# Kernel tuning notes

Measured on AMD Instinct MI355X. Metric: run time of the kernel, lower is better.

The kernel has to match this reference:

```python
import jax, jax.numpy as jnp
import numpy as np

N = 20000       # nodes
C = 64          # channels per irrep
E = 320000      # edges (avg degree 16)
S = 64          # num_species
R = 8           # radial embedding dim
HR = 64         # radial MLP hidden
HEADS = 2       # readout heads
AVG = 16.0      # avg_num_neighbors
SOFT = 2.0      # soft_normalization


def setup_inputs() -> dict:
    key = jax.random.key(0)
    ks = jax.random.split(key, 28)
    g = lambda k, sh, sc=1.0: jax.random.normal(k, sh, dtype=jnp.float32) * sc
    inv = lambda n: 1.0 / float(np.sqrt(n))
    return {
        "edge_vectors": g(ks[0], (E, 3)),
        "node_feats_s": g(ks[1], (N, C)),
        "node_feats_v": g(ks[2], (N, C, 3)),
        "radial_embeddings": g(ks[3], (E, R)),
        "node_species": jax.random.randint(ks[4], (N,), 0, S),
        "senders": jax.random.randint(ks[5], (E,), 0, N),
        "receivers": jax.random.randint(ks[6], (E,), 0, N),
        # residual FullyConnectedTensorProduct(feats, one-hot species) weights
        "W_rs": g(ks[7], (S, C, C), inv(C)),
        "W_rv": g(ks[8], (S, C, C), inv(C)),
        # interaction: linear up, radial MLP (5 TP paths), linear down
        "W_up_s": g(ks[9], (C, C), inv(C)),
        "W_up_v": g(ks[10], (C, C), inv(C)),
        "Wr1": g(ks[11], (R, HR), inv(R)),
        "Wr2": g(ks[12], (HR, 5 * C), inv(HR)),
        "W_down_s": g(ks[13], (C, C), inv(C)),
        "W_down_v": g(ks[14], (C, C), inv(C)),
        # equivariant product basis: per-channel species-indexed symmetric-contraction weights
        "w1s": g(ks[15], (S, C)),
        "w1v": g(ks[16], (S, C)),
        "w2ss": g(ks[17], (S, C)),
        "w2vv": g(ks[18], (S, C)),
        "w2sv": g(ks[19], (S, C)),
        "W_prod_s": g(ks[20], (C, C), inv(C)),
        "W_prod_v": g(ks[21], (C, C), inv(C)),
        # linear readout heads (out_irreps -> 1x0e per head)
        "w_read": g(ks[22], (HEADS, C), inv(C)),
    }


def reference(edge_vectors, node_feats_s, node_feats_v, radial_embeddings,
              node_species, senders, receivers,
              W_rs, W_rv, W_up_s, W_up_v, Wr1, Wr2, W_down_s, W_down_v,
              w1s, w1v, w2ss, w2vv, w2sv, W_prod_s, W_prod_v, w_read):
    n_nodes = node_feats_s.shape[0]
    sp = node_species

    # --- residual connection: FCTP(feats, one-hot(species)) == species-indexed channel mix
    res_s = jnp.einsum('nc,ncd->nd', node_feats_s, W_rs[sp])
    res_v = jnp.einsum('ncx,ncd->ndx', node_feats_v, W_rv[sp])

    # --- InteractionBlock ---
    s_u = node_feats_s @ W_up_s
    v_u = jnp.einsum('ncx,cd->ndx', node_feats_v, W_up_v)
    nrm = jnp.linalg.norm(edge_vectors, axis=-1, keepdims=True)
    u = edge_vectors / jnp.maximum(nrm, 1e-9)  # l=1 spherical harmonic direction [E,3]
    # radial MLP -> per-edge per-channel weights for the 5 CG paths of (0e+1o)x(0e+1o)->0e+1o
    w = (jax.nn.silu(radial_embeddings @ Wr1) @ Wr2).reshape(-1, 5, s_u.shape[1])
    se = s_u[senders]            # [E,C] gather (irregular)
    ve = v_u[senders]            # [E,C,3]
    dot = jnp.einsum('ecx,ex->ec', ve, u)          # 1o x 1o -> 0e
    crs = jnp.cross(ve, u[:, None, :])             # 1o x 1o -> 1o
    m_s = w[:, 0] * se + w[:, 3] * dot
    m_v = (w[:, 1][..., None] * ve
           + w[:, 2][..., None] * u[:, None, :]
           + w[:, 4][..., None] * crs)
    a_s = jax.ops.segment_sum(m_s, receivers, num_segments=n_nodes) / AVG
    a_v = jax.ops.segment_sum(m_v, receivers, num_segments=n_nodes) / AVG
    a_s = a_s @ W_down_s
    a_v = jnp.einsum('ncx,cd->ndx', a_v, W_down_v)

    # --- EquivariantProductBasisBlock: symmetric contraction (correlation<=2), per-channel
    # species-indexed weights, followed by a linear to out_irreps ---
    vv = jnp.sum(a_v * a_v, axis=-1)                                   # 1o (x) 1o -> 0e
    p_s = w1s[sp] * a_s + w2ss[sp] * a_s * a_s + w2vv[sp] * vv
    p_v = w1v[sp][..., None] * a_v + w2sv[sp][..., None] * a_s[..., None] * a_v
    p_s = p_s @ W_prod_s
    p_v = jnp.einsum('ncx,cd->ndx', p_v, W_prod_v)

    # --- soft normalization: phi(n) = 1/(1 + n*sus(n)), n = norm/SOFT ---
    def sus(x):
        return jnp.where(x > 0, jnp.exp(-1.0 / jnp.where(x > 0, x, 1.0)), 0.0)

    def phi(n):
        n = n / SOFT
        return 1.0 / (1.0 + n * sus(n))

    f_s = p_s * phi(jnp.abs(p_s))
    f_v = p_v * phi(jnp.linalg.norm(p_v, axis=-1, keepdims=True))

    # --- residual add ---
    f_s = f_s + res_s
    f_v = f_v + res_v

    # --- readout heads (Linear out_irreps -> 1x0e), stacked on axis=1 ---
    node_out = jnp.einsum('nc,hc->nh', f_s, w_read)
    return (node_out, f_s, f_v)
```

## Files before the change

### kernel.cpp

```cpp
#include <hip/hip_runtime.h>

#define N_NODES 20000
#define C 64
#define E_EDGES 320000
#define S_SPEC 64
#define R_DIM 8
#define HR 64
#define HEADS 2
#define TE 128
#define NT (E_EDGES/TE)
#define HPAD 68
#define INV_AVG (1.0f/16.0f)

#define FS_OFF 40000
#define FV_OFF 1320000

typedef short bf16x4 __attribute__((ext_vector_type(4)));
typedef float f32x4  __attribute__((ext_vector_type(4)));

__device__ __forceinline__ unsigned short f2bf(float f){
  unsigned u = __float_as_uint(f);
  u += 0x7fffu + ((u >> 16) & 1u);
  return (unsigned short)(u >> 16);
}
__device__ __forceinline__ float bf2f(unsigned short b){
  return __uint_as_float(((unsigned)b) << 16);
}
__device__ __forceinline__ float phi_f(float x){
  float n = x * 0.5f;
  float s = (n > 0.0f) ? expf(-1.0f/n) : 0.0f;
  return 1.0f / (1.0f + n * s);
}

__global__ __launch_bounds__(256) void wr2t_kernel(const float* __restrict__ Wr2,
                                                   unsigned short* __restrict__ wr2t){
  int idx = blockIdx.x*256 + threadIdx.x;
  int n = idx >> 6, k = idx & 63;
  wr2t[idx] = f2bf(Wr2[k*320 + n] * INV_AVG);
}

__global__ __launch_bounds__(256) void node_up_kernel(
    const float* __restrict__ fs, const float* __restrict__ fv,
    const float* __restrict__ Wus, const float* __restrict__ Wuv,
    ushort4* __restrict__ suv){
  const int ni = threadIdx.x >> 6;
  const int d  = threadIdx.x & 63;
  const int n  = blockIdx.x*4 + ni;
  __shared__ float s_l[4][C];
  __shared__ float v_l[4][3][C];
  s_l[ni][d] = fs[n*C + d];
  #pragma unroll
  for (int x = 0; x < 3; ++x) v_l[ni][x][d] = fv[(n*C + d)*3 + x];
  __syncthreads();
  float as = 0.f, a0 = 0.f, a1 = 0.f, a2 = 0.f;
  #pragma unroll 4
  for (int c = 0; c < C; ++c){
    float wsv = Wus[c*C + d];
    float wvv = Wuv[c*C + d];
    as += s_l[ni][c] * wsv;
    a0 += v_l[ni][0][c] * wvv;
    a1 += v_l[ni][1][c] * wvv;
    a2 += v_l[ni][2][c] * wvv;
  }
  ushort4 o;
  o.x = f2bf(as); o.y = f2bf(a0); o.z = f2bf(a1); o.w = f2bf(a2);
  suv[(size_t)n*C + d] = o;
}

__global__ __launch_bounds__(256) void hist_kernel(const int* __restrict__ rcv, int* __restrict__ count){
  int e = blockIdx.x*256 + threadIdx.x;
  atomicAdd(&count[rcv[e]], 1);
}

__global__ __launch_bounds__(1024) void scan_kernel(const int* __restrict__ count, int* __restrict__ cursor){
  __shared__ int sums[1024];
  const int t = threadIdx.x;
  const int base = t*20;
  int s = 0;
  #pragma unroll 4
  for (int i = 0; i < 20; ++i){ int idx = base+i; if (idx < N_NODES) s += count[idx]; }
  sums[t] = s;
  __syncthreads();
  for (int off = 1; off < 1024; off <<= 1){
    int v = (t >= off) ? sums[t-off] : 0;
    __syncthreads();
    sums[t] += v;
    __syncthreads();
  }
  int run = (t > 0) ? sums[t-1] : 0;
  for (int i = 0; i < 20; ++i){
    int idx = base+i;
    if (idx < N_NODES){ cursor[idx] = run; run += count[idx]; }
  }
}

__global__ __launch_bounds__(256) void scatter_kernel(
    const int* __restrict__ snd, const int* __restrict__ rcv,
    const float* __restrict__ ev, const float* __restrict__ re,
    int* __restrict__ cursor,
    int* __restrict__ snd_s, int* __restrict__ rcv_s,
    float4* __restrict__ u_s, float* __restrict__ re_s){
  int e = blockIdx.x*256 + threadIdx.x;
  int r = rcv[e];
  int pos = atomicAdd(&cursor[r], 1);
  snd_s[pos] = snd[e];
  rcv_s[pos] = r;
  float x = ev[e*3+0], y = ev[e*3+1], z = ev[e*3+2];
  float nr = sqrtf(x*x + y*y + z*z);
  float inv = 1.0f / fmaxf(nr, 1e-9f);
  float4 u4; u4.x = x*inv; u4.y = y*inv; u4.z = z*inv; u4.w = 0.f;
  u_s[pos] = u4;
  const float4* rp = (const float4*)&re[(size_t)e*R_DIM];
  float4 ra = rp[0], rb = rp[1];
  float4* op = (float4*)&re_s[(size_t)pos*R_DIM];
  op[0] = ra; op[1] = rb;
}

__global__ __launch_bounds__(512, 4) void edge_kernel(
    const float4* __restrict__ u_s, const float* __restrict__ re_s,
    const int* __restrict__ snd_s, const int* __restrict__ rcv_s,
    const float* __restrict__ Wr1, const unsigned short* __restrict__ wr2t,
    const ushort4* __restrict__ suv,
    float* __restrict__ a_s, float* __restrict__ a_v)
{
  __shared__ __align__(16) float Wr1_l[R_DIM*HR];
  __shared__ __align__(16) unsigned short Wr2T_l[320*HPAD];
  __shared__ __align__(16) unsigned short h_l[TE*HPAD];
  __shared__ __align__(16) float4 u_l[TE];
  __shared__ int snd_l[TE];
  __shared__ int rcv_l[TE];

  const int t = threadIdx.x;
  const int lane = t & 63;
  const int w = t >> 6;
  int b = blockIdx.x;
  int xcd = b & 7, idx = b >> 3;
  const int q = NT >> 3, r = NT & 7;
  int tile = (xcd < r ? xcd*(q+1) : r*(q+1) + (xcd-r)*q) + idx;
  const int e0 = tile * TE;

  Wr1_l[t] = Wr1[t];
  #pragma unroll
  for (int j = 0; j < 10; ++j){
    int i4 = t + 512*j;
    ushort4 v4 = ((const ushort4*)wr2t)[i4];
    int el = i4*4; int n = el >> 6, k = el & 63;
    *(ushort4*)&Wr2T_l[n*HPAD + k] = v4;
  }
  if (t < TE){
    int e = e0 + t;
    u_l[t] = u_s[e];
    snd_l[t] = snd_s[e];
    rcv_l[t] = rcv_s[e];
  }
  __syncthreads();

  const int cl = lane & 15;
  const int ebase = w*16 + (lane >> 4)*4;
  ushort4 gv[4][4];
  #pragma unroll
  for (int i = 0; i < 4; ++i){
    const ushort4* sp_ = &suv[(size_t)snd_l[ebase + i]*C];
    #pragma unroll
    for (int k2 = 0; k2 < 4; ++k2) gv[i][k2] = sp_[k2*16 + cl];
  }

  {
    int e = t & 127, qh = t >> 7;
    const float4* rp = (const float4*)&re_s[(size_t)(e0 + e)*R_DIM];
    float4 ra = rp[0], rb = rp[1];
    unsigned short hh[16];
    #pragma unroll
    for (int kk = 0; kk < 16; ++kk){
      int k = qh*16 + kk;
      float acc = ra.x*Wr1_l[0*HR+k] + ra.y*Wr1_l[1*HR+k] + ra.z*Wr1_l[2*HR+k] + ra.w*Wr1_l[3*HR+k]
                + rb.x*Wr1_l[4*HR+k] + rb.y*Wr1_l[5*HR+k] + rb.z*Wr1_l[6*HR+k] + rb.w*Wr1_l[7*HR+k];
      hh[kk] = f2bf(acc / (1.0f + expf(-acc)));
    }
    #pragma unroll
    for (int j4 = 0; j4 < 4; ++j4)
      *(ushort4*)&h_l[e*HPAD + qh*16 + j4*4] = *(ushort4*)&hh[j4*4];
  }
  __syncthreads();

  f32x4 acc[20];
  #pragma unroll
  for (int cf = 0; cf < 20; ++cf) acc[cf] = (f32x4){0.f,0.f,0.f,0.f};
  {
    const int arow = (w*16 + (lane & 15))*HPAD;
    const int koff = 4*(lane >> 4);
    #pragma unroll
    for (int kt = 0; kt < 4; ++kt){
      bf16x4 af = *(const bf16x4*)&h_l[arow + kt*16 + koff];
      #pragma unroll
      for (int cf = 0; cf < 20; ++cf){
        bf16x4 bf = *(const bf16x4*)&Wr2T_l[(cf*16 + (lane & 15))*HPAD + kt*16 + koff];
        acc[cf] = __builtin_amdgcn_mfma_f32_16x16x16bf16_1k(af, bf, acc[cf], 0, 0, 0);
      }
    }
  }

  {
    float ms[4], mv0[4], mv1[4], mv2[4];
    #pragma unroll
    for (int k2 = 0; k2 < 4; ++k2){ ms[k2]=0.f; mv0[k2]=0.f; mv1[k2]=0.f; mv2[k2]=0.f; }
    int cur = rcv_l[ebase];
    #pragma unroll
    for (int i = 0; i < 4; ++i){
      int el = ebase + i;
      int rc = rcv_l[el];
      if (rc != cur){
        #pragma unroll
        for (int k2 = 0; k2 < 4; ++k2){
          int c = k2*16 + cl;
          unsafeAtomicAdd(&a_s[cur*C + c],       ms[k2]);
          unsafeAtomicAdd(&a_v[(cur*3+0)*C + c], mv0[k2]);
          unsafeAtomicAdd(&a_v[(cur*3+1)*C + c], mv1[k2]);
          unsafeAtomicAdd(&a_v[(cur*3+2)*C + c], mv2[k2]);
          ms[k2]=0.f; mv0[k2]=0.f; mv1[k2]=0.f; mv2[k2]=0.f;
        }
        cur = rc;
      }
      float u0 = u_l[el].x, u1 = u_l[el].y, u2 = u_l[el].z;
      #pragma unroll
      for (int k2 = 0; k2 < 4; ++k2){
        float se  = bf2f(gv[i][k2].x);
        float ve0 = bf2f(gv[i][k2].y);
        float ve1 = bf2f(gv[i][k2].z);
        float ve2 = bf2f(gv[i][k2].w);
        float w0 = acc[0*4+k2][i];
        float w1 = acc[1*4+k2][i];
        float w2 = acc[2*4+k2][i];
        float w3 = acc[3*4+k2][i];
        float w4 = acc[4*4+k2][i];
        float dt  = ve0*u0 + ve1*u1 + ve2*u2;
        float cr0 = ve1*u2 - ve2*u1;
        float cr1 = ve2*u0 - ve0*u2;
        float cr2 = ve0*u1 - ve1*u0;
        ms[k2]  += w0*se + w3*dt;
        mv0[k2] += w1*ve0 + w2*u0 + w4*cr0;
        mv1[k2] += w1*ve1 + w2*u1 + w4*cr1;
        mv2[k2] += w1*ve2 + w2*u2 + w4*cr2;
      }
    }
    #pragma unroll
    for (int k2 = 0; k2 < 4; ++k2){
      int c = k2*16 + cl;
      unsafeAtomicAdd(&a_s[cur*C + c],       ms[k2]);
      unsafeAtomicAdd(&a_v[(cur*3+0)*C + c], mv0[k2]);
      unsafeAtomicAdd(&a_v[(cur*3+1)*C + c], mv1[k2]);
      unsafeAtomicAdd(&a_v[(cur*3+2)*C + c], mv2[k2]);
    }
  }
}

__global__ __launch_bounds__(256) void node_post_kernel(
    const float* __restrict__ a_s, const float* __restrict__ a_v,
    const float* __restrict__ fs_in, const float* __restrict__ fv_in,
    const int* __restrict__ species,
    const float* __restrict__ W_rs, const float* __restrict__ W_rv,
    const float* __restrict__ W_ds, const float* __restrict__ W_dv,
    const float* __restrict__ w1s, const float* __restrict__ w1v,
    const float* __restrict__ w2ss, const float* __restrict__ w2vv, const float* __restrict__ w2sv,
    const float* __restrict__ W_ps, const float* __restrict__ W_pv,
    const float* __restrict__ w_read, float* __restrict__ out)
{
  const int ni = threadIdx.x >> 6;
  const int d  = threadIdx.x & 63;
  const int n  = blockIdx.x*4 + ni;
  const int sp = species[n];
  __shared__ float as_l[4][C];
  __shared__ float av_l[4][3][C];
  __shared__ float si_l[4][C];
  __shared__ float vi_l[4][3][C];
  as_l[ni][d] = a_s[n*C + d];
  #pragma unroll
  for (int x=0;x<3;x++) av_l[ni][x][d] = a_v[(n*3+x)*C + d];
  si_l[ni][d] = fs_in[n*C + d];
  #pragma unroll
  for (int x=0;x<3;x++) vi_l[ni][x][d] = fv_in[(n*C + d)*3 + x];
  __syncthreads();
  const float* Wrs_p = W_rs + sp*C*C;
  const float* Wrv_p = W_rv + sp*C*C;
  float bs=0, bv0=0, bv1=0, bv2=0, rs=0, rv0=0, rv1=0, rv2=0;
  for (int c=0;c<C;++c){
    float wds = W_ds[c*C+d], wdv = W_dv[c*C+d];
    float wrs = Wrs_p[c*C+d], wrv = Wrv_p[c*C+d];
    bs  += as_l[ni][c]*wds;
    bv0 += av_l[ni][0][c]*wdv; bv1 += av_l[ni][1][c]*wdv; bv2 += av_l[ni][2][c]*wdv;
    rs  += si_l[ni][c]*wrs;
    rv0 += vi_l[ni][0][c]*wrv; rv1 += vi_l[ni][1][c]*wrv; rv2 += vi_l[ni][2][c]*wrv;
  }
  float vv = bv0*bv0 + bv1*bv1 + bv2*bv2;
  float ps  = w1s[sp*C+d]*bs + w2ss[sp*C+d]*bs*bs + w2vv[sp*C+d]*vv;
  float c1v = w1v[sp*C+d], c2sv = w2sv[sp*C+d];
  float pv0 = c1v*bv0 + c2sv*bs*bv0;
  float pv1 = c1v*bv1 + c2sv*bs*bv1;
  float pv2 = c1v*bv2 + c2sv*bs*bv2;
  __syncthreads();
  as_l[ni][d] = ps; av_l[ni][0][d]=pv0; av_l[ni][1][d]=pv1; av_l[ni][2][d]=pv2;
  __syncthreads();
  float qs=0, qv0=0, qv1=0, qv2=0;
  for (int c=0;c<C;++c){
    float wps = W_ps[c*C+d], wpv = W_pv[c*C+d];
    qs  += as_l[ni][c]*wps;
    qv0 += av_l[ni][0][c]*wpv; qv1 += av_l[ni][1][c]*wpv; qv2 += av_l[ni][2][c]*wpv;
  }
  float fsv = qs * phi_f(fabsf(qs)) + rs;
  float nv = sqrtf(qv0*qv0 + qv1*qv1 + qv2*qv2);
  float ph = phi_f(nv);
  float fv0 = qv0*ph + rv0;
  float fv1 = qv1*ph + rv1;
  float fv2 = qv2*ph + rv2;
  out[FS_OFF + n*C + d] = fsv;
  float* fvo = &out[FV_OFF + (size_t)(n*C + d)*3];
  fvo[0]=fv0; fvo[1]=fv1; fvo[2]=fv2;
  #pragma unroll
  for (int h=0; h<HEADS; ++h){
    float r = fsv * w_read[h*C + d];
    #pragma unroll
    for (int off=32; off>0; off>>=1) r += __shfl_down(r, off);
    if (d == 0) out[n*HEADS + h] = r;
  }
}

extern "C" void kernel_launch(void* const* d_in, const int* in_sizes, int n_in,
                              void* d_out, int out_size, void* d_ws, size_t ws_size,
                              hipStream_t stream)
{
  const float* ev   = (const float*)d_in[0];
  const float* nfs  = (const float*)d_in[1];
  const float* nfv  = (const float*)d_in[2];
  const float* re   = (const float*)d_in[3];
  const int*   spec = (const int*)d_in[4];
  const int*   snd  = (const int*)d_in[5];
  const int*   rcv  = (const int*)d_in[6];
  const float* W_rs = (const float*)d_in[7];
  const float* W_rv = (const float*)d_in[8];
  const float* Wus  = (const float*)d_in[9];
  const float* Wuv  = (const float*)d_in[10];
  const float* Wr1  = (const float*)d_in[11];
  const float* Wr2  = (const float*)d_in[12];
  const float* Wds  = (const float*)d_in[13];
  const float* Wdv  = (const float*)d_in[14];
  const float* w1s  = (const float*)d_in[15];
  const float* w1v  = (const float*)d_in[16];
  const float* w2ss = (const float*)d_in[17];
  const float* w2vv = (const float*)d_in[18];
  const float* w2sv = (const float*)d_in[19];
  const float* Wps  = (const float*)d_in[20];
  const float* Wpv  = (const float*)d_in[21];
  const float* wrd  = (const float*)d_in[22];

  float* out = (float*)d_out;
  float* ws  = (float*)d_ws;
  ushort4* suv  = (ushort4*)ws;
  float*   a_s  = ws + 2560000;
  float*   a_v  = ws + 3840000;
  int*    count = (int*)(ws + 7680000);
  int*    cursr = (int*)(ws + 7700000);
  int*    snd_s = (int*)(ws + 7720000);
  int*    rcv_s = (int*)(ws + 8040000);
  float4* u_s   = (float4*)(ws + 8360000);
  float*  re_s  = ws + 9640000;
  unsigned short* wr2t = (unsigned short*)(ws + 12200000);

  hipMemsetAsync(a_s, 0, (size_t)5120000*sizeof(float), stream);
  hipMemsetAsync(count, 0, (size_t)N_NODES*sizeof(int), stream);

  wr2t_kernel<<<(320*64)/256, 256, 0, stream>>>(Wr2, wr2t);
  node_up_kernel<<<N_NODES/4, 256, 0, stream>>>(nfs, nfv, Wus, Wuv, suv);
  hist_kernel<<<E_EDGES/256, 256, 0, stream>>>(rcv, count);
  scan_kernel<<<1, 1024, 0, stream>>>(count, cursr);
  scatter_kernel<<<E_EDGES/256, 256, 0, stream>>>(snd, rcv, ev, re, cursr,
                                                  snd_s, rcv_s, u_s, re_s);
  edge_kernel<<<NT, 512, 0, stream>>>(u_s, re_s, snd_s, rcv_s, Wr1, wr2t,
                                      suv, a_s, a_v);
  node_post_kernel<<<N_NODES/4, 256, 0, stream>>>(a_s, a_v, nfs, nfv, spec,
      W_rs, W_rv, Wds, Wdv, w1s, w1v, w2ss, w2vv, w2sv, Wps, Wpv, wrd, out);
}
```

Before: 433.9 us.

## Aggregate edge messages per receiver segment in LDS before global atomics

Edges within a tile, already sorted by receiver, are grouped into receiver segments with a block-wide prefix scan. Each thread reduces its partial messages into a shared-memory slot per segment using LDS atomics, and one flush then issues a single global atomic per segment and channel. Segments past the slot limit still fall back to direct global atomics. The radial MLP hidden layer is now computed directly in registers as MFMA A-fragments, dropping the h_l staging buffer and one barrier. In exchange the kernel adds a serial scan with several barriers, extra LDS (about 24 KB of accumulators) that may lower occupancy, and LDS atomic contention.

Result: faster. 411.2 us (-5.2%).

```diff
diff --git a/kernel.cpp b/kernel.cpp
--- a/kernel.cpp
+++ b/kernel.cpp
@@ -10,6 +10,7 @@
 #define TE 128
 #define NT (E_EDGES/TE)
 #define HPAD 68
+#define NSLOT 24
 #define INV_AVG (1.0f/16.0f)
 
 #define FS_OFF 40000
@@ -125,10 +126,14 @@
 {
   __shared__ __align__(16) float Wr1_l[R_DIM*HR];
   __shared__ __align__(16) unsigned short Wr2T_l[320*HPAD];
-  __shared__ __align__(16) unsigned short h_l[TE*HPAD];
+  __shared__ __align__(16) float re_l[TE][9];
   __shared__ __align__(16) float4 u_l[TE];
   __shared__ int snd_l[TE];
   __shared__ int rcv_l[TE];
+  __shared__ int scan_l[TE];
+  __shared__ int slot_rcv[NSLOT];
+  __shared__ float accum[NSLOT][4][C];
+  __shared__ int nslots_s;
 
   const int t = threadIdx.x;
   const int lane = t & 63;
@@ -147,6 +152,13 @@
     int el = i4*4; int n = el >> 6, k = el & 63;
     *(ushort4*)&Wr2T_l[n*HPAD + k] = v4;
   }
+  #pragma unroll
+  for (int i2 = 0; i2 < 2; ++i2){
+    int idx2 = t + 512*i2;
+    re_l[idx2 >> 3][idx2 & 7] = re_s[(size_t)e0*R_DIM + idx2];
+  }
+  #pragma unroll
+  for (int z = t; z < NSLOT*4*C; z += 512) ((float*)accum)[z] = 0.f;
   if (t < TE){
     int e = e0 + t;
     u_l[t] = u_s[e];
@@ -155,71 +167,98 @@
   }
   __syncthreads();
 
-  const int cl = lane & 15;
-  const int ebase = w*16 + (lane >> 4)*4;
-  ushort4 gv[4][4];
-  #pragma unroll
-  for (int i = 0; i < 4; ++i){
-    const ushort4* sp_ = &suv[(size_t)snd_l[ebase + i]*C];
-    #pragma unroll
-    for (int k2 = 0; k2 < 4; ++k2) gv[i][k2] = sp_[k2*16 + cl];
-  }
-
+  if (t < TE) scan_l[t] = (t == 0) ? 1 : (rcv_l[t] != rcv_l[t-1] ? 1 : 0);
+  __syncthreads();
+  for (int off = 1; off < TE; off <<= 1){
+    int v = 0;
+    if (t < TE && t >= off) v = scan_l[t-off];
+    __syncthreads();
+    if (t < TE) scan_l[t] += v;
+    __syncthreads();
+  }
+  if (t == 0) nslots_s = scan_l[TE-1];
+  if (t < TE){
+    bool flag = (t == 0) || (rcv_l[t] != rcv_l[t-1]);
+    int slot = scan_l[t] - 1;
+    if (flag && slot < NSLOT) slot_rcv[slot] = rcv_l[t];
+  }
+  __syncthreads();
+
+  const int arow = w*16 + (lane & 15);
+  const int koff = 4*(lane >> 4);
+  bf16x4 ha[4];
   {
-    int e = t & 127, qh = t >> 7;
-    const float4* rp = (const float4*)&re_s[(size_t)(e0 + e)*R_DIM];
-    float4 ra = rp[0], rb = rp[1];
-    unsigned short hh[16];
-    #pragma unroll
-    for (int kk = 0; kk < 16; ++kk){
-      int k = qh*16 + kk;
-      float acc = ra.x*Wr1_l[0*HR+k] + ra.y*Wr1_l[1*HR+k] + ra.z*Wr1_l[2*HR+k] + ra.w*Wr1_l[3*HR+k]
-                + rb.x*Wr1_l[4*HR+k] + rb.y*Wr1_l[5*HR+k] + rb.z*Wr1_l[6*HR+k] + rb.w*Wr1_l[7*HR+k];
-      hh[kk] = f2bf(acc / (1.0f + expf(-acc)));
-    }
-    #pragma unroll
-    for (int j4 = 0; j4 < 4; ++j4)
-      *(ushort4*)&h_l[e*HPAD + qh*16 + j4*4] = *(ushort4*)&hh[j4*4];
-  }
-  __syncthreads();
+    const float* rr = re_l[arow];
+    #pragma unroll
+    for (int kt = 0; kt < 4; ++kt){
+      short4 tmp;
+      #pragma unroll
+      for (int j = 0; j < 4; ++j){
+        int k = kt*16 + koff + j;
+        float acc = rr[0]*Wr1_l[0*HR+k] + rr[1]*Wr1_l[1*HR+k] + rr[2]*Wr1_l[2*HR+k] + rr[3]*Wr1_l[3*HR+k]
+                  + rr[4]*Wr1_l[4*HR+k] + rr[5]*Wr1_l[5*HR+k] + rr[6]*Wr1_l[6*HR+k] + rr[7]*Wr1_l[7*HR+k];
+        float sil = acc / (1.0f + expf(-acc));
+        ((unsigned short*)&tmp)[j] = f2bf(sil);
+      }
+      ha[kt] = *(bf16x4*)&tmp;
+    }
+  }
 
   f32x4 acc[20];
   #pragma unroll
   for (int cf = 0; cf < 20; ++cf) acc[cf] = (f32x4){0.f,0.f,0.f,0.f};
+  #pragma unroll
+  for (int kt = 0; kt < 4; ++kt){
+    bf16x4 af = ha[kt];
+    #pragma unroll
+    for (int cf = 0; cf < 20; ++cf){
+      bf16x4 bf = *(const bf16x4*)&Wr2T_l[(cf*16 + (lane & 15))*HPAD + kt*16 + koff];
+      acc[cf] = __builtin_amdgcn_mfma_f32_16x16x16bf16_1k(af, bf, acc[cf], 0, 0, 0);
+    }
+  }
+
   {
-    const int arow = (w*16 + (lane & 15))*HPAD;
-    const int koff = 4*(lane >> 4);
-    #pragma unroll
-    for (int kt = 0; kt < 4; ++kt){
-      bf16x4 af = *(const bf16x4*)&h_l[arow + kt*16 + koff];
+    const int cl = lane & 15;
+    const int ebase = w*16 + (lane >> 4)*4;
+    ushort4 gv[4][4];
+    #pragma unroll
+    for (int i = 0; i < 4; ++i){
+      const ushort4* sp_ = &suv[(size_t)snd_l[ebase + i]*C];
       #pragma unroll
-      for (int cf = 0; cf < 20; ++cf){
-        bf16x4 bf = *(const bf16x4*)&Wr2T_l[(cf*16 + (lane & 15))*HPAD + kt*16 + koff];
-        acc[cf] = __builtin_amdgcn_mfma_f32_16x16x16bf16_1k(af, bf, acc[cf], 0, 0, 0);
-      }
-    }
-  }
-
-  {
+      for (int k2 = 0; k2 < 4; ++k2) gv[i][k2] = sp_[k2*16 + cl];
+    }
     float ms[4], mv0[4], mv1[4], mv2[4];
     #pragma unroll
     for (int k2 = 0; k2 < 4; ++k2){ ms[k2]=0.f; mv0[k2]=0.f; mv1[k2]=0.f; mv2[k2]=0.f; }
     int cur = rcv_l[ebase];
+    int cur_slot = scan_l[ebase] - 1;
     #pragma unroll
     for (int i = 0; i < 4; ++i){
       int el = ebase + i;
       int rc = rcv_l[el];
       if (rc != cur){
-        #pragma unroll
-        for (int k2 = 0; k2 < 4; ++k2){
-          int c = k2*16 + cl;
-          unsafeAtomicAdd(&a_s[cur*C + c],       ms[k2]);
-          unsafeAtomicAdd(&a_v[(cur*3+0)*C + c], mv0[k2]);
-          unsafeAtomicAdd(&a_v[(cur*3+1)*C + c], mv1[k2]);
-          unsafeAtomicAdd(&a_v[(cur*3+2)*C + c], mv2[k2]);
-          ms[k2]=0.f; mv0[k2]=0.f; mv1[k2]=0.f; mv2[k2]=0.f;
+        if (cur_slot < NSLOT){
+          #pragma unroll
+          for (int k2 = 0; k2 < 4; ++k2){
+            int c = k2*16 + cl;
+            atomicAdd(&accum[cur_slot][0][c], ms[k2]);
+            atomicAdd(&accum[cur_slot][1][c], mv0[k2]);
+            atomicAdd(&accum[cur_slot][2][c], mv1[k2]);
+            atomicAdd(&accum[cur_slot][3][c], mv2[k2]);
+            ms[k2]=0.f; mv0[k2]=0.f; mv1[k2]=0.f; mv2[k2]=0.f;
+          }
+        } else {
+          #pragma unroll
+          for (int k2 = 0; k2 < 4; ++k2){
+            int c = k2*16 + cl;
+            unsafeAtomicAdd(&a_s[cur*C + c],       ms[k2]);
+            unsafeAtomicAdd(&a_v[(cur*3+0)*C + c], mv0[k2]);
+            unsafeAtomicAdd(&a_v[(cur*3+1)*C + c], mv1[k2]);
+            unsafeAtomicAdd(&a_v[(cur*3+2)*C + c], mv2[k2]);
+            ms[k2]=0.f; mv0[k2]=0.f; mv1[k2]=0.f; mv2[k2]=0.f;
+          }
         }
-        cur = rc;
+        cur = rc; cur_slot = scan_l[el] - 1;
       }
       float u0 = u_l[el].x, u1 = u_l[el].y, u2 = u_l[el].z;
       #pragma unroll
@@ -243,13 +282,36 @@
         mv2[k2] += w1*ve2 + w2*u2 + w4*cr2;
       }
     }
-    #pragma unroll
-    for (int k2 = 0; k2 < 4; ++k2){
-      int c = k2*16 + cl;
-      unsafeAtomicAdd(&a_s[cur*C + c],       ms[k2]);
-      unsafeAtomicAdd(&a_v[(cur*3+0)*C + c], mv0[k2]);
-      unsafeAtomicAdd(&a_v[(cur*3+1)*C + c], mv1[k2]);
-      unsafeAtomicAdd(&a_v[(cur*3+2)*C + c], mv2[k2]);
+    if (cur_slot < NSLOT){
+      #pragma unroll
+      for (int k2 = 0; k2 < 4; ++k2){
+        int c = k2*16 + cl;
+        atomicAdd(&accum[cur_slot][0][c], ms[k2]);
+        atomicAdd(&accum[cur_slot][1][c], mv0[k2]);
+        atomicAdd(&accum[cur_slot][2][c], mv1[k2]);
+        atomicAdd(&accum[cur_slot][3][c], mv2[k2]);
+      }
+    } else {
+      #pragma unroll
+      for (int k2 = 0; k2 < 4; ++k2){
+        int c = k2*16 + cl;
+        unsafeAtomicAdd(&a_s[cur*C + c],       ms[k2]);
+        unsafeAtomicAdd(&a_v[(cur*3+0)*C + c], mv0[k2]);
+        unsafeAtomicAdd(&a_v[(cur*3+1)*C + c], mv1[k2]);
+        unsafeAtomicAdd(&a_v[(cur*3+2)*C + c], mv2[k2]);
+      }
+    }
+  }
+  __syncthreads();
+
+  {
+    int ns = nslots_s; if (ns > NSLOT) ns = NSLOT;
+    for (int v = t; v < ns*256; v += 512){
+      int slot = v >> 8, f = (v >> 6) & 3, c = v & 63;
+      int rr = slot_rcv[slot];
+      float val = accum[slot][f][c];
+      if (f == 0) unsafeAtomicAdd(&a_s[rr*C + c], val);
+      else        unsafeAtomicAdd(&a_v[(rr*3 + (f-1))*C + c], val);
     }
   }
 }
```

## Compute radial hidden activations in MFMA register layout, drop edge-tile LDS staging

Applied to the files above, without the earlier changes.

Each lane now computes the SiLU radial hidden values it needs straight into MFMA A-operand registers, instead of writing them to an LDS tile and reading them back. Per-edge unit vectors, senders and receivers also load into registers rather than shared memory. One barrier goes away, and the sender feature gather moves after the MFMA loop. The smaller shared-memory footprint allows launch bounds to request 6 blocks per SM instead of 4, at the cost of redundant first-layer MLP work across lanes and tighter register limits that may cause spills.

Measured after the change: 653.2 us. 1.51x slower.

```diff
diff --git a/kernel.cpp b/kernel.cpp
--- a/kernel.cpp
+++ b/kernel.cpp
@@ -116,7 +116,7 @@
   op[0] = ra; op[1] = rb;
 }
 
-__global__ __launch_bounds__(512, 4) void edge_kernel(
+__global__ __launch_bounds__(512, 6) void edge_kernel(
     const float4* __restrict__ u_s, const float* __restrict__ re_s,
     const int* __restrict__ snd_s, const int* __restrict__ rcv_s,
     const float* __restrict__ Wr1, const unsigned short* __restrict__ wr2t,
@@ -125,10 +125,6 @@
 {
   __shared__ __align__(16) float Wr1_l[R_DIM*HR];
   __shared__ __align__(16) unsigned short Wr2T_l[320*HPAD];
-  __shared__ __align__(16) unsigned short h_l[TE*HPAD];
-  __shared__ __align__(16) float4 u_l[TE];
-  __shared__ int snd_l[TE];
-  __shared__ int rcv_l[TE];
 
   const int t = threadIdx.x;
   const int lane = t & 63;
@@ -147,68 +143,67 @@
     int el = i4*4; int n = el >> 6, k = el & 63;
     *(ushort4*)&Wr2T_l[n*HPAD + k] = v4;
   }
-  if (t < TE){
-    int e = e0 + t;
-    u_l[t] = u_s[e];
-    snd_l[t] = snd_s[e];
-    rcv_l[t] = rcv_s[e];
-  }
-  __syncthreads();
-
+
+  const int arow = w*16 + (lane & 15);
+  const int koff = 4*(lane >> 4);
   const int cl = lane & 15;
   const int ebase = w*16 + (lane >> 4)*4;
-  ushort4 gv[4][4];
+  float4 ra = ((const float4*)&re_s[(size_t)(e0 + arow)*R_DIM])[0];
+  float4 rb = ((const float4*)&re_s[(size_t)(e0 + arow)*R_DIM])[1];
+  float4 u4[4];
+  int sn4[4], rc4[4];
   #pragma unroll
   for (int i = 0; i < 4; ++i){
-    const ushort4* sp_ = &suv[(size_t)snd_l[ebase + i]*C];
-    #pragma unroll
-    for (int k2 = 0; k2 < 4; ++k2) gv[i][k2] = sp_[k2*16 + cl];
-  }
-
-  {
-    int e = t & 127, qh = t >> 7;
-    const float4* rp = (const float4*)&re_s[(size_t)(e0 + e)*R_DIM];
-    float4 ra = rp[0], rb = rp[1];
-    unsigned short hh[16];
-    #pragma unroll
-    for (int kk = 0; kk < 16; ++kk){
-      int k = qh*16 + kk;
+    int e = e0 + ebase + i;
+    u4[i] = u_s[e];
+    sn4[i] = snd_s[e];
+    rc4[i] = rcv_s[e];
+  }
+  __syncthreads();
+
+  bf16x4 ha[4];
+  #pragma unroll
+  for (int kt = 0; kt < 4; ++kt){
+    short4 tmp;
+    #pragma unroll
+    for (int j = 0; j < 4; ++j){
+      int k = kt*16 + koff + j;
       float acc = ra.x*Wr1_l[0*HR+k] + ra.y*Wr1_l[1*HR+k] + ra.z*Wr1_l[2*HR+k] + ra.w*Wr1_l[3*HR+k]
                 + rb.x*Wr1_l[4*HR+k] + rb.y*Wr1_l[5*HR+k] + rb.z*Wr1_l[6*HR+k] + rb.w*Wr1_l[7*HR+k];
-      hh[kk] = f2bf(acc / (1.0f + expf(-acc)));
-    }
-    #pragma unroll
-    for (int j4 = 0; j4 < 4; ++j4)
-      *(ushort4*)&h_l[e*HPAD + qh*16 + j4*4] = *(ushort4*)&hh[j4*4];
-  }
-  __syncthreads();
+      float sil = acc / (1.0f + expf(-acc));
+      ((unsigned short*)&tmp)[j] = f2bf(sil);
+    }
+    ha[kt] = *(bf16x4*)&tmp;
+  }
 
   f32x4 acc[20];
   #pragma unroll
   for (int cf = 0; cf < 20; ++cf) acc[cf] = (f32x4){0.f,0.f,0.f,0.f};
+  #pragma unroll
+  for (int kt = 0; kt < 4; ++kt){
+    bf16x4 af = ha[kt];
+    #pragma unroll
+    for (int cf = 0; cf < 20; ++cf){
+      bf16x4 bf = *(const bf16x4*)&Wr2T_l[(cf*16 + (lane & 15))*HPAD + kt*16 + koff];
+      acc[cf] = __builtin_amdgcn_mfma_f32_16x16x16bf16_1k(af, bf, acc[cf], 0, 0, 0);
+    }
+  }
+
   {
-    const int arow = (w*16 + (lane & 15))*HPAD;
-    const int koff = 4*(lane >> 4);
-    #pragma unroll
-    for (int kt = 0; kt < 4; ++kt){
-      bf16x4 af = *(const bf16x4*)&h_l[arow + kt*16 + koff];
+    ushort4 gv[4][4];
+    #pragma unroll
+    for (int i = 0; i < 4; ++i){
+      const ushort4* sp_ = &suv[(size_t)sn4[i]*C];
       #pragma unroll
-      for (int cf = 0; cf < 20; ++cf){
-        bf16x4 bf = *(const bf16x4*)&Wr2T_l[(cf*16 + (lane & 15))*HPAD + kt*16 + koff];
-        acc[cf] = __builtin_amdgcn_mfma_f32_16x16x16bf16_1k(af, bf, acc[cf], 0, 0, 0);
-      }
-    }
-  }
-
-  {
+      for (int k2 = 0; k2 < 4; ++k2) gv[i][k2] = sp_[k2*16 + cl];
+    }
     float ms[4], mv0[4], mv1[4], mv2[4];
     #pragma unroll
     for (int k2 = 0; k2 < 4; ++k2){ ms[k2]=0.f; mv0[k2]=0.f; mv1[k2]=0.f; mv2[k2]=0.f; }
-    int cur = rcv_l[ebase];
+    int cur = rc4[0];
     #pragma unroll
     for (int i = 0; i < 4; ++i){
-      int el = ebase + i;
-      int rc = rcv_l[el];
+      int rc = rc4[i];
       if (rc != cur){
         #pragma unroll
         for (int k2 = 0; k2 < 4; ++k2){
@@ -221,7 +216,7 @@
         }
         cur = rc;
       }
-      float u0 = u_l[el].x, u1 = u_l[el].y, u2 = u_l[el].z;
+      float u0 = u4[i].x, u1 = u4[i].y, u2 = u4[i].z;
       #pragma unroll
       for (int k2 = 0; k2 < 4; ++k2){
         float se  = bf2f(gv[i][k2].x);
```
